# Optimization experiments

Measured on AMD Instinct MI355X. Metric: run time of the kernel, lower is better.

The kernel has to match this reference:

```python
import jax, jax.numpy as jnp
import numpy as np

EPS = 1e-8


def setup_inputs() -> dict:
    key = jax.random.key(0)
    ks = jax.random.split(key, 8)
    B, N, D = 8, 1024, 256
    x = jax.random.normal(ks[0], (B, N, D), dtype=jnp.float32)
    y = jax.random.normal(ks[1], (B, N, D), dtype=jnp.float32)
    coords = jax.random.normal(ks[2], (N, N, 6), dtype=jnp.float32)
    # xavier-ish init for U, kaiming-ish for S1/S2
    U = jax.random.normal(ks[3], (D, D), dtype=jnp.float32) * (1.0 / np.sqrt(D))
    S1 = jax.random.normal(ks[4], (D, 1), dtype=jnp.float32)
    S2 = jax.random.normal(ks[5], (D, 1), dtype=jnp.float32)
    gating = jnp.asarray(1.0, dtype=jnp.float32)
    h_temp = jnp.asarray(0.1, dtype=jnp.float32)
    p_temp = jnp.asarray(1.0, dtype=jnp.float32)
    # trunc_normal_(a=0, b=1): std-normal truncated to [0, 1]
    pos_emb = jax.random.truncated_normal(ks[6], 0.0, 1.0, (N, 6, 1)).astype(jnp.float32)
    return {"x": x, "y": y, "coords": coords, "U": U, "S1": S1, "S2": S2,
            "gating": gating, "h_temp": h_temp, "p_temp": p_temp, "pos_emb": pos_emb}


def _spectral(x, U, S):
    # x @ U.T @ diag(|S|) @ U  ==  ((x @ U.T) * |S|) @ U
    s = jnp.abs(S[:, 0])
    return ((x @ U.T) * s) @ U


def reference(x, y, coords, U, S1, S2, gating, h_temp, p_temp, pos_emb):
    B, N, D = x.shape
    scale = D ** (-0.5)
    xs = jnp.stack([_spectral(x, U, S1), _spectral(x, U, S2)], axis=1)  # [B,2,N,D]
    # patch attention scores: [B,2,N,N]
    patch_score = jax.nn.softmax(jnp.einsum('bknd,bmd->bknm', xs, y) * scale, axis=-1)
    # positional scores, shared across batch and the 2 spectral branches: [N,N]
    pos_logits = -jnp.abs(p_temp) * jnp.einsum('nmc,ncq->nm', coords, pos_emb)
    pos_score = jax.nn.softmax(pos_logits, axis=-1)
    g = jax.nn.sigmoid(gating)
    attn = (1.0 - g) * patch_score + g * pos_score[None, None]  # [B,2,N,N]
    # entropy over key axis -> [B,N,2]
    entropy = jnp.sum(-attn * jnp.log(attn + EPS), axis=-1).transpose(0, 2, 1)
    hmap = 2.0 - 2.0 * jax.nn.sigmoid(h_temp * entropy)  # [B,N,2]
    fgbg = hmap[..., 0] >= hmap[..., 1]
    route = jax.lax.stop_gradient(
        jnp.stack([fgbg, ~fgbg], axis=-1).astype(hmap.dtype))  # [B,N,2]
    heat_map = jnp.sum(hmap * route, axis=-1, keepdims=True)  # [B,N,1]
    attn_sel = jnp.sum(attn * route.transpose(0, 2, 1)[..., None], axis=1)  # [B,N,N]
    out = attn_sel @ y  # [B,N,D]
    return (out, heat_map)
```

## Files before the change

kernel.cpp:

```cpp
#include <hip/hip_runtime.h>
#include <hip/hip_bf16.h>
#include <stdint.h>


#define NB 8
#define NN_ 1024
#define ND 256

typedef __bf16 bf16x8 __attribute__((ext_vector_type(8)));
typedef __bf16 bf16x4 __attribute__((ext_vector_type(4)));
typedef float f32x4 __attribute__((ext_vector_type(4)));

__device__ inline void gl_lds(const __bf16* g, __bf16* l) {
    auto gp = (const __attribute__((address_space(1))) uint32_t*)(uintptr_t)g;
    auto lp = (__attribute__((address_space(3))) uint32_t*)(uintptr_t)l;
    __builtin_amdgcn_global_load_lds(gp, lp, 16, 0, 0);
}

__device__ inline float wred_sum(float v) {
#pragma unroll
    for (int o = 32; o; o >>= 1) v += __shfl_xor(v, o, 64);
    return v;
}
__device__ inline float wred_max(float v) {
#pragma unroll
    for (int o = 32; o; o >>= 1) v = fmaxf(v, __shfl_xor(v, o, 64));
    return v;
}

__global__ __launch_bounds__(256) void prep_kernel(
    const float* __restrict__ coords, const float* __restrict__ pos_emb,
    const float* __restrict__ p_temp, const float* __restrict__ x,
    const float* __restrict__ y, const float* __restrict__ U,
    const float* __restrict__ S1, const float* __restrict__ S2,
    float* __restrict__ posS, __bf16* __restrict__ Xh, __bf16* __restrict__ Xl,
    __bf16* __restrict__ yt, __bf16* __restrict__ Yh, __bf16* __restrict__ Yl,
    __bf16* __restrict__ Mh, __bf16* __restrict__ Ml) {
    __shared__ char sm[9216 + 64];
    const int bid = blockIdx.x;
    const int tid = threadIdx.x;

    if (bid < 1024) {
        float* red = (float*)sm;
        const int n = bid;
        const float pt = -fabsf(p_temp[0]);
        float pe[6];
#pragma unroll
        for (int c = 0; c < 6; ++c) pe[c] = pos_emb[n * 6 + c];
        const float* cr = coords + (long)n * NN_ * 6;
        float l[4];
#pragma unroll
        for (int j = 0; j < 4; ++j) {
            const int m = j * 256 + tid;
            const float2* cp = (const float2*)(cr + (long)m * 6);
            float2 c0 = cp[0], c1 = cp[1], c2 = cp[2];
            l[j] = pt * (c0.x * pe[0] + c0.y * pe[1] + c1.x * pe[2] +
                         c1.y * pe[3] + c2.x * pe[4] + c2.y * pe[5]);
        }
        float mx = fmaxf(fmaxf(l[0], l[1]), fmaxf(l[2], l[3]));
        mx = wred_max(mx);
        __syncthreads();
        if ((tid & 63) == 0) red[tid >> 6] = mx;
        __syncthreads();
        mx = fmaxf(fmaxf(red[0], red[1]), fmaxf(red[2], red[3]));
        float e[4], s = 0.f;
#pragma unroll
        for (int j = 0; j < 4; ++j) { e[j] = __expf(l[j] - mx); s += e[j]; }
        s = wred_sum(s);
        __syncthreads();
        if ((tid & 63) == 0) red[4 + (tid >> 6)] = s;
        __syncthreads();
        s = red[4] + red[5] + red[6] + red[7];
        const float inv = 1.f / s;
#pragma unroll
        for (int j = 0; j < 4; ++j)
            posS[(long)n * NN_ + j * 256 + tid] = e[j] * inv;
    } else if (bid < 1536) {
        const int n4 = NB * NN_ * ND / 4;
        int i = (bid - 1024) * 256 + tid;
        for (; i < n4; i += 512 * 256) {
            float4 v = ((const float4*)x)[i];
            bf16x4 h, l;
            h[0] = (__bf16)v.x; l[0] = (__bf16)(v.x - (float)h[0]);
            h[1] = (__bf16)v.y; l[1] = (__bf16)(v.y - (float)h[1]);
            h[2] = (__bf16)v.z; l[2] = (__bf16)(v.z - (float)h[2]);
            h[3] = (__bf16)v.w; l[3] = (__bf16)(v.w - (float)h[3]);
            ((bf16x4*)Xh)[i] = h;
            ((bf16x4*)Xl)[i] = l;
        }
    } else if (bid < 2048) {
        __bf16 (*t)[72] = (__bf16(*)[72])sm;
        const int rem = bid - 1536;
        const int b = rem >> 6;
        const int m0 = (rem & 15) * 64, d0 = ((rem >> 4) & 3) * 64;
        const int c = tid & 15;
        const int r = tid >> 4;
#pragma unroll
        for (int p = 0; p < 4; ++p) {
            const int row = r + p * 16;
            const long gi = ((long)b * NN_ + m0 + row) * ND + d0 + c * 4;
            float4 v = *(const float4*)(y + gi);
            bf16x4 h, l;
            h[0] = (__bf16)v.x; l[0] = (__bf16)(v.x - (float)h[0]);
            h[1] = (__bf16)v.y; l[1] = (__bf16)(v.y - (float)h[1]);
            h[2] = (__bf16)v.z; l[2] = (__bf16)(v.z - (float)h[2]);
            h[3] = (__bf16)v.w; l[3] = (__bf16)(v.w - (float)h[3]);
            *(bf16x4*)(Yh + gi) = h;
            *(bf16x4*)(Yl + gi) = l;
            t[c * 4 + 0][row] = h[0]; t[c * 4 + 1][row] = h[1];
            t[c * 4 + 2][row] = h[2]; t[c * 4 + 3][row] = h[3];
        }
        __syncthreads();
#pragma unroll
        for (int p = 0; p < 4; ++p) {
            const int d = r + p * 16;
            bf16x4 o;
            o[0] = t[d][c * 4 + 0]; o[1] = t[d][c * 4 + 1];
            o[2] = t[d][c * 4 + 2]; o[3] = t[d][c * 4 + 3];
            *(bf16x4*)(yt + ((long)b * ND + d0 + d) * NN_ + m0 + c * 4) = o;
        }
    } else {
        const int n = bid - 2048, j = tid;
        float a1 = 0.f, a2 = 0.f;
        for (int c = 0; c < ND; ++c) {
            const float un = U[c * ND + n];
            const float uj = U[c * ND + j];
            a1 = fmaf(fabsf(S1[c]) * un, uj, a1);
            a2 = fmaf(fabsf(S2[c]) * un, uj, a2);
        }
        const __bf16 h1 = (__bf16)a1, h2 = (__bf16)a2;
        Mh[n * ND + j] = h1;           Ml[n * ND + j] = (__bf16)(a1 - (float)h1);
        Mh[65536 + n * ND + j] = h2;   Ml[65536 + n * ND + j] = (__bf16)(a2 - (float)h2);
    }
}

__global__ __launch_bounds__(256) void mgemm_xs(
    const __bf16* __restrict__ Ah, const __bf16* __restrict__ Al,
    const __bf16* __restrict__ Bh, const __bf16* __restrict__ Bl,
    __bf16* __restrict__ Ch, __bf16* __restrict__ Cl,
    int M, int N, int K, long sB1, long sC) {
    constexpr int BM = 128, BK = 32, BN = 64;
    __shared__ __bf16 As[2 * BM * BK];
    __shared__ __bf16 Bs[2 * BN * BK];

    const int z = blockIdx.z;
    Bh += (long)z * sB1; Bl += (long)z * sB1;

    const int tid = threadIdx.x;
    const int bm = blockIdx.y * BM, bn = blockIdx.x * BN;
    const int wave = tid >> 6, lane = tid & 63;
    const int wm = wave >> 1, wn = wave & 1;
    const int quad = lane >> 4, l16 = lane & 15;

    f32x4 acc[4][2];
#pragma unroll
    for (int i = 0; i < 4; ++i)
#pragma unroll
        for (int j = 0; j < 2; ++j) acc[i][j] = (f32x4){0.f, 0.f, 0.f, 0.f};

    const int srow = lane >> 2;
    const int slot = lane & 3;

    for (int k0 = 0; k0 < K; k0 += BK) {
        __syncthreads();
#pragma unroll
        for (int i = 0; i < 2; ++i) {
            const int r0 = wave * 32 + i * 16;
            const int row = r0 + srow;
            const int chunk = slot ^ ((row >> 1) & 3);
            const long g = (long)(bm + row) * K + k0 + chunk * 8;
            gl_lds(Ah + g, &As[r0 * 32]);
            gl_lds(Al + g, &As[BM * BK + r0 * 32]);
        }
        {
            const int r0 = wave * 16;
            const int row = r0 + srow;
            const int chunk = slot ^ ((row >> 1) & 3);
            const long g = (long)(bn + row) * K + k0 + chunk * 8;
            gl_lds(Bh + g, &Bs[r0 * 32]);
            gl_lds(Bl + g, &Bs[BN * BK + r0 * 32]);
        }
        __syncthreads();

        bf16x8 a_h[4], a_l[4], b_h[2], b_l[2];
#pragma unroll
        for (int mi = 0; mi < 4; ++mi) {
            const int row = wm * 64 + mi * 16 + l16;
            const int off = row * 32 + ((quad ^ ((row >> 1) & 3)) * 8);
            a_h[mi] = *(const bf16x8*)&As[off];
            a_l[mi] = *(const bf16x8*)&As[BM * BK + off];
        }
#pragma unroll
        for (int ni = 0; ni < 2; ++ni) {
            const int row = wn * 32 + ni * 16 + l16;
            const int off = row * 32 + ((quad ^ ((row >> 1) & 3)) * 8);
            b_h[ni] = *(const bf16x8*)&Bs[off];
            b_l[ni] = *(const bf16x8*)&Bs[BN * BK + off];
        }
#pragma unroll
        for (int mi = 0; mi < 4; ++mi)
#pragma unroll
            for (int ni = 0; ni < 2; ++ni) {
                acc[mi][ni] = __builtin_amdgcn_mfma_f32_16x16x32_bf16(
                    a_h[mi], b_h[ni], acc[mi][ni], 0, 0, 0);
                acc[mi][ni] = __builtin_amdgcn_mfma_f32_16x16x32_bf16(
                    a_h[mi], b_l[ni], acc[mi][ni], 0, 0, 0);
                acc[mi][ni] = __builtin_amdgcn_mfma_f32_16x16x32_bf16(
                    a_l[mi], b_h[ni], acc[mi][ni], 0, 0, 0);
            }
    }

    Ch += (long)z * sC; Cl += (long)z * sC;
#pragma unroll
    for (int mi = 0; mi < 4; ++mi) {
        const int row0 = bm + wm * 64 + mi * 16 + quad * 4;
#pragma unroll
        for (int ni = 0; ni < 2; ++ni) {
            const int col = bn + wn * 32 + ni * 16 + l16;
#pragma unroll
            for (int r = 0; r < 4; ++r) {
                const float v = acc[mi][ni][r];
                const long idx = (long)(row0 + r) * N + col;
                const __bf16 h = (__bf16)v;
                Ch[idx] = h;
                Cl[idx] = (__bf16)(v - (float)h);
            }
        }
    }
}

__global__ __launch_bounds__(256) void mgemm_sc(
    const __bf16* __restrict__ Ah, const __bf16* __restrict__ Al,
    const __bf16* __restrict__ Bh, const __bf16* __restrict__ Bl,
    float* __restrict__ C, int N, int K,
    long sA1, long sA2, long sB1, long sC, float alpha) {
    constexpr int BM = 128, BK = 32, BN = 128;
    __shared__ __bf16 As[2][2 * BM * BK];
    __shared__ __bf16 Bs[2][2 * BN * BK];

    const int z = blockIdx.z;
    const long aoff = (long)(z >> 1) * sA1 + (long)(z & 1) * sA2;
    const long boff = (long)(z >> 1) * sB1;
    Ah += aoff; Al += aoff;
    Bh += boff; Bl += boff;

    const int tid = threadIdx.x;
    const int bm = blockIdx.y * BM, bn = blockIdx.x * BN;
    const int wave = tid >> 6, lane = tid & 63;
    const int wm = wave >> 1, wn = wave & 1;
    const int quad = lane >> 4, l16 = lane & 15;

    f32x4 acc[4][4];
#pragma unroll
    for (int i = 0; i < 4; ++i)
#pragma unroll
        for (int j = 0; j < 4; ++j) acc[i][j] = (f32x4){0.f, 0.f, 0.f, 0.f};

    const int srow = lane >> 2;
    const int slot = lane & 3;

    auto stage = [&](int sel, int k0) {
#pragma unroll
        for (int i = 0; i < 2; ++i) {
            const int r0 = wave * 32 + i * 16;
            const int row = r0 + srow;
            const int chunk = slot ^ ((row >> 1) & 3);
            const long ga = (long)(bm + row) * K + k0 + chunk * 8;
            gl_lds(Ah + ga, &As[sel][r0 * 32]);
            gl_lds(Al + ga, &As[sel][BM * BK + r0 * 32]);
            const long gb = (long)(bn + row) * K + k0 + chunk * 8;
            gl_lds(Bh + gb, &Bs[sel][r0 * 32]);
            gl_lds(Bl + gb, &Bs[sel][BN * BK + r0 * 32]);
        }
    };

    stage(0, 0);
    __syncthreads();
    int cur = 0;
    for (int k0 = 0; k0 < K; k0 += BK) {
        if (k0 + BK < K) stage(cur ^ 1, k0 + BK);

        bf16x8 a_h[4], a_l[4], b_h[4], b_l[4];
#pragma unroll
        for (int mi = 0; mi < 4; ++mi) {
            const int row = wm * 64 + mi * 16 + l16;
            const int off = row * 32 + ((quad ^ ((row >> 1) & 3)) * 8);
            a_h[mi] = *(const bf16x8*)&As[cur][off];
            a_l[mi] = *(const bf16x8*)&As[cur][BM * BK + off];
        }
#pragma unroll
        for (int ni = 0; ni < 4; ++ni) {
            const int row = wn * 64 + ni * 16 + l16;
            const int off = row * 32 + ((quad ^ ((row >> 1) & 3)) * 8);
            b_h[ni] = *(const bf16x8*)&Bs[cur][off];
            b_l[ni] = *(const bf16x8*)&Bs[cur][BN * BK + off];
        }
#pragma unroll
        for (int mi = 0; mi < 4; ++mi)
#pragma unroll
            for (int ni = 0; ni < 4; ++ni) {
                acc[mi][ni] = __builtin_amdgcn_mfma_f32_16x16x32_bf16(
                    a_h[mi], b_h[ni], acc[mi][ni], 0, 0, 0);
                acc[mi][ni] = __builtin_amdgcn_mfma_f32_16x16x32_bf16(
                    a_h[mi], b_l[ni], acc[mi][ni], 0, 0, 0);
                acc[mi][ni] = __builtin_amdgcn_mfma_f32_16x16x32_bf16(
                    a_l[mi], b_h[ni], acc[mi][ni], 0, 0, 0);
            }

        __syncthreads();
        cur ^= 1;
    }

    C += (long)z * sC;
#pragma unroll
    for (int mi = 0; mi < 4; ++mi) {
        const int row0 = bm + wm * 64 + mi * 16 + quad * 4;
#pragma unroll
        for (int ni = 0; ni < 4; ++ni) {
            const int col = bn + wn * 64 + ni * 16 + l16;
#pragma unroll
            for (int r = 0; r < 4; ++r)
                __builtin_nontemporal_store(acc[mi][ni][r] * alpha,
                                            &C[(long)(row0 + r) * NN_ + col]);
        }
    }
}

__global__ __launch_bounds__(256, 8) void blendsm_kernel(
    const float* __restrict__ S, const float* __restrict__ pos,
    const float* __restrict__ gating, const float* __restrict__ h_temp,
    __bf16* __restrict__ P, float* __restrict__ heat) {
    const int b = blockIdx.x & 7;
    const int n = (blockIdx.x >> 3) * 4 + (threadIdx.x >> 6);
    const int lane = threadIdx.x & 63;

    const float g = 1.f / (1.f + __expf(-gating[0]));
    const float cg = 1.f - g;
    const float ht = h_temp[0];

    const float* r0p = S + ((long)(b * 2 + 0) * NN_ + n) * NN_;
    const float* r1p = S + ((long)(b * 2 + 1) * NN_ + n) * NN_;

    f32x4 a0[4], a1[4];
#pragma unroll
    for (int j = 0; j < 4; ++j) {
        a0[j] = __builtin_nontemporal_load((const f32x4*)(r0p + j * 256 + lane * 4));
        a1[j] = __builtin_nontemporal_load((const f32x4*)(r1p + j * 256 + lane * 4));
    }
    float m0 = -3.4e38f, m1 = -3.4e38f;
#pragma unroll
    for (int j = 0; j < 4; ++j) {
        m0 = fmaxf(m0, fmaxf(fmaxf(a0[j][0], a0[j][1]), fmaxf(a0[j][2], a0[j][3])));
        m1 = fmaxf(m1, fmaxf(fmaxf(a1[j][0], a1[j][1]), fmaxf(a1[j][2], a1[j][3])));
    }
    m0 = wred_max(m0); m1 = wred_max(m1);
    float s0 = 0.f, s1 = 0.f;
#pragma unroll
    for (int j = 0; j < 4; ++j) {
        a0[j][0] = __expf(a0[j][0] - m0); a0[j][1] = __expf(a0[j][1] - m0);
        a0[j][2] = __expf(a0[j][2] - m0); a0[j][3] = __expf(a0[j][3] - m0);
        s0 += a0[j][0] + a0[j][1] + a0[j][2] + a0[j][3];
        a1[j][0] = __expf(a1[j][0] - m1); a1[j][1] = __expf(a1[j][1] - m1);
        a1[j][2] = __expf(a1[j][2] - m1); a1[j][3] = __expf(a1[j][3] - m1);
        s1 += a1[j][0] + a1[j][1] + a1[j][2] + a1[j][3];
    }
    s0 = wred_sum(s0); s1 = wred_sum(s1);
    const float i0 = 1.f / s0, i1 = 1.f / s1;
    const float* pr = pos + (long)n * NN_;
    float e0 = 0.f, e1 = 0.f;
#pragma unroll
    for (int j = 0; j < 4; ++j) {
        const f32x4 pv = *(const f32x4*)(pr + j * 256 + lane * 4);
        a0[j][0] = cg * a0[j][0] * i0 + g * pv[0];
        a0[j][1] = cg * a0[j][1] * i0 + g * pv[1];
        a0[j][2] = cg * a0[j][2] * i0 + g * pv[2];
        a0[j][3] = cg * a0[j][3] * i0 + g * pv[3];
        a1[j][0] = cg * a1[j][0] * i1 + g * pv[0];
        a1[j][1] = cg * a1[j][1] * i1 + g * pv[1];
        a1[j][2] = cg * a1[j][2] * i1 + g * pv[2];
        a1[j][3] = cg * a1[j][3] * i1 + g * pv[3];
        e0 -= a0[j][0] * __logf(a0[j][0] + 1e-8f) + a0[j][1] * __logf(a0[j][1] + 1e-8f) +
              a0[j][2] * __logf(a0[j][2] + 1e-8f) + a0[j][3] * __logf(a0[j][3] + 1e-8f);
        e1 -= a1[j][0] * __logf(a1[j][0] + 1e-8f) + a1[j][1] * __logf(a1[j][1] + 1e-8f) +
              a1[j][2] * __logf(a1[j][2] + 1e-8f) + a1[j][3] * __logf(a1[j][3] + 1e-8f);
    }
    e0 = wred_sum(e0); e1 = wred_sum(e1);
    const float hm0 = 2.f - 2.f / (1.f + __expf(-ht * e0));
    const float hm1 = 2.f - 2.f / (1.f + __expf(-ht * e1));
    const bool fg = (hm0 >= hm1);
    if (lane == 0) heat[(long)b * NN_ + n] = fg ? hm0 : hm1;
    __bf16* prow = P + ((long)b * NN_ + n) * NN_;
#pragma unroll
    for (int j = 0; j < 4; ++j) {
        const f32x4 v = fg ? a0[j] : a1[j];
        bf16x4 o;
        o[0] = (__bf16)v[0]; o[1] = (__bf16)v[1];
        o[2] = (__bf16)v[2]; o[3] = (__bf16)v[3];
        *(bf16x4*)(prow + j * 256 + lane * 4) = o;
    }
}

__global__ __launch_bounds__(256) void pv_gemm(
    const __bf16* __restrict__ A, const __bf16* __restrict__ Bm,
    float* __restrict__ C) {
    constexpr int BM = 128, BK = 32, BN = 64;
    __shared__ __bf16 As[2][BM * BK];
    __shared__ __bf16 Bs[2][BN * BK];

    const int z = blockIdx.z;
    A  += (long)z * NN_ * NN_;
    Bm += (long)z * ND * NN_;
    C  += (long)z * NN_ * ND;

    const int tid = threadIdx.x;
    const int bm = blockIdx.y * BM, bn = blockIdx.x * BN;
    const int wave = tid >> 6, lane = tid & 63;
    const int wm = wave >> 1, wn = wave & 1;
    const int quad = lane >> 4, l16 = lane & 15;
    const int srow = lane >> 2, slot = lane & 3;

    f32x4 acc[4][2];
#pragma unroll
    for (int i = 0; i < 4; ++i)
#pragma unroll
        for (int j = 0; j < 2; ++j) acc[i][j] = (f32x4){0.f, 0.f, 0.f, 0.f};

    auto stage = [&](int sel, int k0) {
#pragma unroll
        for (int i = 0; i < 2; ++i) {
            const int r0 = wave * 32 + i * 16;
            const int row = r0 + srow;
            const int chunk = slot ^ ((row >> 1) & 3);
            gl_lds(A + (long)(bm + row) * NN_ + k0 + chunk * 8, &As[sel][r0 * 32]);
        }
        {
            const int r0 = wave * 16;
            const int row = r0 + srow;
            const int chunk = slot ^ ((row >> 1) & 3);
            gl_lds(Bm + (long)(bn + row) * NN_ + k0 + chunk * 8, &Bs[sel][r0 * 32]);
        }
    };

    stage(0, 0);
    __syncthreads();
    int cur = 0;
    for (int k0 = 0; k0 < NN_; k0 += BK) {
        if (k0 + BK < NN_) stage(cur ^ 1, k0 + BK);

        bf16x8 a[4], bb[2];
#pragma unroll
        for (int mi = 0; mi < 4; ++mi) {
            const int row = wm * 64 + mi * 16 + l16;
            const int off = row * 32 + ((quad ^ ((row >> 1) & 3)) * 8);
            a[mi] = *(const bf16x8*)&As[cur][off];
        }
#pragma unroll
        for (int ni = 0; ni < 2; ++ni) {
            const int row = wn * 32 + ni * 16 + l16;
            const int off = row * 32 + ((quad ^ ((row >> 1) & 3)) * 8);
            bb[ni] = *(const bf16x8*)&Bs[cur][off];
        }
#pragma unroll
        for (int mi = 0; mi < 4; ++mi)
#pragma unroll
            for (int ni = 0; ni < 2; ++ni)
                acc[mi][ni] = __builtin_amdgcn_mfma_f32_16x16x32_bf16(
                    a[mi], bb[ni], acc[mi][ni], 0, 0, 0);

        __syncthreads();
        cur ^= 1;
    }

#pragma unroll
    for (int mi = 0; mi < 4; ++mi) {
        const int row0 = bm + wm * 64 + mi * 16 + quad * 4;
#pragma unroll
        for (int ni = 0; ni < 2; ++ni) {
            const int col = bn + wn * 32 + ni * 16 + l16;
#pragma unroll
            for (int r = 0; r < 4; ++r)
                __builtin_nontemporal_store(acc[mi][ni][r],
                                            &C[(long)(row0 + r) * ND + col]);
        }
    }
}

extern "C" void kernel_launch(void* const* d_in, const int* in_sizes, int n_in,
                              void* d_out, int out_size, void* d_ws, size_t ws_size,
                              hipStream_t stream) {
    const float* x      = (const float*)d_in[0];
    const float* y      = (const float*)d_in[1];
    const float* coords = (const float*)d_in[2];
    const float* U      = (const float*)d_in[3];
    const float* S1p    = (const float*)d_in[4];
    const float* S2p    = (const float*)d_in[5];
    const float* gating = (const float*)d_in[6];
    const float* h_temp = (const float*)d_in[7];
    const float* p_temp = (const float*)d_in[8];
    const float* pos_emb= (const float*)d_in[9];

    float* out  = (float*)d_out;
    float* heat = out + (long)NB * NN_ * ND;

    char* ws = (char*)d_ws;
    const long MB = 1 << 20;
    float*  Sf  = (float*)(ws);
    float*  pos = (float*)(ws + 64 * MB);
    __bf16* Xh  = (__bf16*)(ws + 68 * MB);
    __bf16* Xl  = (__bf16*)(ws + 72 * MB);
    __bf16* XSh = (__bf16*)(ws + 76 * MB);
    __bf16* XSl = (__bf16*)(ws + 84 * MB);
    __bf16* yt  = (__bf16*)(ws + 92 * MB);
    __bf16* Yh  = (__bf16*)(ws + 96 * MB);
    __bf16* Yl  = (__bf16*)(ws + 100 * MB);
    __bf16* Mh  = (__bf16*)(ws + 104 * MB);
    __bf16* Ml  = Mh + 2 * 65536;
    __bf16* Pb  = (__bf16*)(ws + 76 * MB);

    const long ND2 = (long)NN_ * ND;
    const long BND = (long)NB * ND2;

    prep_kernel<<<dim3(2304), 256, 0, stream>>>(
        coords, pos_emb, p_temp, x, y, U, S1p, S2p,
        pos, Xh, Xl, yt, Yh, Yl, Mh, Ml);

    mgemm_xs<<<dim3(4, 64, 2), 256, 0, stream>>>(
        Xh, Xl, Mh, Ml, XSh, XSl, NB * NN_, ND, ND, 65536, BND);

    mgemm_sc<<<dim3(8, 8, NB * 2), 256, 0, stream>>>(
        XSh, XSl, Yh, Yl, Sf, NN_, ND,
        ND2, BND, ND2, (long)NN_ * NN_, 0.0625f);

    blendsm_kernel<<<dim3(2048), 256, 0, stream>>>(
        Sf, pos, gating, h_temp, Pb, heat);

    pv_gemm<<<dim3(4, 8, 8), 256, 0, stream>>>(Pb, yt, out);

    (void)in_sizes; (void)n_in; (void)out_size; (void)ws_size;
}
```

Baseline: 210.2 us.

## Remap score GEMM blocks per XCD, drop double buffering and nontemporal hints

The score GEMM now launches as a flat 1D grid and remaps block IDs so that each of the 8 XCDs handles two complete (batch, branch) score matrices, which keeps A/B tile reuse inside one XCD's L2. Its LDS double buffering is replaced by a single buffer with two barriers per K step, halving LDS use so more blocks can be resident. The cost is that the next tile's loads no longer overlap the current tile's MFMAs. Nontemporal stores and loads are also swapped for plain ones on the score matrix and output, so the score writes can stay in cache for the softmax/blend kernel that reads them next.

```diff
diff --git a/kernel.cpp b/kernel.cpp
--- a/kernel.cpp
+++ b/kernel.cpp
@@ -235,17 +235,23 @@
     float* __restrict__ C, int N, int K,
     long sA1, long sA2, long sB1, long sC, float alpha) {
     constexpr int BM = 128, BK = 32, BN = 128;
-    __shared__ __bf16 As[2][2 * BM * BK];
-    __shared__ __bf16 Bs[2][2 * BN * BK];
-
-    const int z = blockIdx.z;
+    __shared__ __bf16 As[2 * BM * BK];
+    __shared__ __bf16 Bs[2 * BN * BK];
+
+    const int bid = blockIdx.x;
+    const int xcd = bid & 7;
+    const int j   = bid >> 3;
+    const int z   = 2 * xcd + (j >> 6);
+    const int t   = j & 63;
+    const int bm  = (t >> 3) * BM;
+    const int bn  = (t & 7) * BN;
+
     const long aoff = (long)(z >> 1) * sA1 + (long)(z & 1) * sA2;
     const long boff = (long)(z >> 1) * sB1;
     Ah += aoff; Al += aoff;
     Bh += boff; Bl += boff;
 
     const int tid = threadIdx.x;
-    const int bm = blockIdx.y * BM, bn = blockIdx.x * BN;
     const int wave = tid >> 6, lane = tid & 63;
     const int wm = wave >> 1, wn = wave & 1;
     const int quad = lane >> 4, l16 = lane & 15;
@@ -254,46 +260,41 @@
 #pragma unroll
     for (int i = 0; i < 4; ++i)
 #pragma unroll
-        for (int j = 0; j < 4; ++j) acc[i][j] = (f32x4){0.f, 0.f, 0.f, 0.f};
+        for (int jj = 0; jj < 4; ++jj) acc[i][jj] = (f32x4){0.f, 0.f, 0.f, 0.f};
 
     const int srow = lane >> 2;
     const int slot = lane & 3;
 
-    auto stage = [&](int sel, int k0) {
+    for (int k0 = 0; k0 < K; k0 += BK) {
+        __syncthreads();
 #pragma unroll
         for (int i = 0; i < 2; ++i) {
             const int r0 = wave * 32 + i * 16;
             const int row = r0 + srow;
             const int chunk = slot ^ ((row >> 1) & 3);
             const long ga = (long)(bm + row) * K + k0 + chunk * 8;
-            gl_lds(Ah + ga, &As[sel][r0 * 32]);
-            gl_lds(Al + ga, &As[sel][BM * BK + r0 * 32]);
+            gl_lds(Ah + ga, &As[r0 * 32]);
+            gl_lds(Al + ga, &As[BM * BK + r0 * 32]);
             const long gb = (long)(bn + row) * K + k0 + chunk * 8;
-            gl_lds(Bh + gb, &Bs[sel][r0 * 32]);
-            gl_lds(Bl + gb, &Bs[sel][BN * BK + r0 * 32]);
-        }
-    };
-
-    stage(0, 0);
-    __syncthreads();
-    int cur = 0;
-    for (int k0 = 0; k0 < K; k0 += BK) {
-        if (k0 + BK < K) stage(cur ^ 1, k0 + BK);
+            gl_lds(Bh + gb, &Bs[r0 * 32]);
+            gl_lds(Bl + gb, &Bs[BN * BK + r0 * 32]);
+        }
+        __syncthreads();
 
         bf16x8 a_h[4], a_l[4], b_h[4], b_l[4];
 #pragma unroll
         for (int mi = 0; mi < 4; ++mi) {
             const int row = wm * 64 + mi * 16 + l16;
             const int off = row * 32 + ((quad ^ ((row >> 1) & 3)) * 8);
-            a_h[mi] = *(const bf16x8*)&As[cur][off];
-            a_l[mi] = *(const bf16x8*)&As[cur][BM * BK + off];
+            a_h[mi] = *(const bf16x8*)&As[off];
+            a_l[mi] = *(const bf16x8*)&As[BM * BK + off];
         }
 #pragma unroll
         for (int ni = 0; ni < 4; ++ni) {
             const int row = wn * 64 + ni * 16 + l16;
             const int off = row * 32 + ((quad ^ ((row >> 1) & 3)) * 8);
-            b_h[ni] = *(const bf16x8*)&Bs[cur][off];
-            b_l[ni] = *(const bf16x8*)&Bs[cur][BN * BK + off];
+            b_h[ni] = *(const bf16x8*)&Bs[off];
+            b_l[ni] = *(const bf16x8*)&Bs[BN * BK + off];
         }
 #pragma unroll
         for (int mi = 0; mi < 4; ++mi)
@@ -306,9 +307,6 @@
                 acc[mi][ni] = __builtin_amdgcn_mfma_f32_16x16x32_bf16(
                     a_l[mi], b_h[ni], acc[mi][ni], 0, 0, 0);
             }
-
-        __syncthreads();
-        cur ^= 1;
     }
 
     C += (long)z * sC;
@@ -320,8 +318,7 @@
             const int col = bn + wn * 64 + ni * 16 + l16;
 #pragma unroll
             for (int r = 0; r < 4; ++r)
-                __builtin_nontemporal_store(acc[mi][ni][r] * alpha,
-                                            &C[(long)(row0 + r) * NN_ + col]);
+                C[(long)(row0 + r) * NN_ + col] = acc[mi][ni][r] * alpha;
         }
     }
 }
@@ -344,8 +341,8 @@
     f32x4 a0[4], a1[4];
 #pragma unroll
     for (int j = 0; j < 4; ++j) {
-        a0[j] = __builtin_nontemporal_load((const f32x4*)(r0p + j * 256 + lane * 4));
-        a1[j] = __builtin_nontemporal_load((const f32x4*)(r1p + j * 256 + lane * 4));
+        a0[j] = *(const f32x4*)(r0p + j * 256 + lane * 4);
+        a1[j] = *(const f32x4*)(r1p + j * 256 + lane * 4);
     }
     float m0 = -3.4e38f, m1 = -3.4e38f;
 #pragma unroll
@@ -479,8 +476,7 @@
             const int col = bn + wn * 32 + ni * 16 + l16;
 #pragma unroll
             for (int r = 0; r < 4; ++r)
-                __builtin_nontemporal_store(acc[mi][ni][r],
-                                            &C[(long)(row0 + r) * ND + col]);
+                C[(long)(row0 + r) * ND + col] = acc[mi][ni][r];
         }
     }
 }
@@ -527,7 +523,7 @@
     mgemm_xs<<<dim3(4, 64, 2), 256, 0, stream>>>(
         Xh, Xl, Mh, Ml, XSh, XSl, NB * NN_, ND, ND, 65536, BND);
 
-    mgemm_sc<<<dim3(8, 8, NB * 2), 256, 0, stream>>>(
+    mgemm_sc<<<dim3(1024), 256, 0, stream>>>(
         XSh, XSl, Yh, Yl, Sf, NN_, ND,
         ND2, BND, ND2, (long)NN_ * NN_, 0.0625f);
 
```

Measured after the change: 202.1 us. -3.8%, faster.
